# Kernel optimization log

Measured on AMD Instinct MI355X. Metric: run time of the kernel, lower is better.

Reference implementation:

```python
import jax, jax.numpy as jnp
import numpy as np

POOL = 7        # pool_size
NUM_ROIS = 128  # num_rois
WINDOW = 4      # window_size


def setup_inputs() -> dict:
    key = jax.random.key(0)
    k1, k2 = jax.random.split(key)
    img = jax.random.normal(k1, (16, 28, 28, 512), dtype=jnp.float32)
    rois = jax.random.uniform(k2, (16, NUM_ROIS * 5), dtype=jnp.float32)
    return {"img": img, "rois": rois}


def _crop_and_resize(image, boxes, crop):
    """tf.image.crop_and_resize (bilinear, extrapolation_value=0) on a single image.
    image: (H, W, C); boxes: (N, 4) normalized (y1, x1, y2, x2). Returns (N, crop, crop, C)."""
    H, W, C = image.shape
    dt = image.dtype
    y1, x1, y2, x2 = boxes[:, 0], boxes[:, 1], boxes[:, 2], boxes[:, 3]
    i = jnp.arange(crop, dtype=dt)
    # sample grid (crop > 1 branch of TF crop_and_resize)
    ys = y1[:, None] * (H - 1) + i[None, :] * ((y2 - y1) * (H - 1) / (crop - 1))[:, None]  # (N, crop)
    xs = x1[:, None] * (W - 1) + i[None, :] * ((x2 - x1) * (W - 1) / (crop - 1))[:, None]  # (N, crop)
    y0f = jnp.floor(ys)
    x0f = jnp.floor(xs)
    ly = ys - y0f  # fractional weights
    lx = xs - x0f
    y0 = jnp.clip(y0f, 0, H - 1).astype(jnp.int32)
    y1i = jnp.clip(y0f + 1, 0, H - 1).astype(jnp.int32)
    x0 = jnp.clip(x0f, 0, W - 1).astype(jnp.int32)
    x1i = jnp.clip(x0f + 1, 0, W - 1).astype(jnp.int32)
    g = lambda yi, xi: image[yi[:, :, None], xi[:, None, :], :]  # (N, crop, crop, C) gather
    tl, tr, bl, br = g(y0, x0), g(y0, x1i), g(y1i, x0), g(y1i, x1i)
    lxb = lx[:, None, :, None]
    lyb = ly[:, :, None, None]
    val = (tl + (tr - tl) * lxb) * (1 - lyb) + (bl + (br - bl) * lxb) * lyb
    # out-of-range samples -> extrapolation_value = 0
    vy = (ys >= 0) & (ys <= H - 1)
    vx = (xs >= 0) & (xs <= W - 1)
    mask = (vy[:, :, None, None] & vx[:, None, :, None]).astype(dt)
    return val * mask


def reference(img, rois):
    B, H, W, C = img.shape  # H=W=28, C=512 per the layer's hardcoded reshape
    r = rois.reshape(-1, 5)[:, 3:]  # (B*num_rois, 2): columns 3,4 -> x1, y1
    x1 = r[:, 0]
    y1 = r[:, 1]
    x2 = x1 + WINDOW / W  # window_size / cols
    y2 = y1 + WINDOW / H  # window_size / rows
    boxes = jnp.stack([y1, x1, y2, x2], axis=-1)  # (B*num_rois, 4)
    # Original tiles img num_rois times but sets box_ind = zeros, so every crop
    # samples from batch element 0's feature map. Reproduce that exactly.
    crops = _crop_and_resize(img[0], boxes, POOL)  # (B*num_rois, POOL, POOL, C)
    return crops.reshape(B, POOL, POOL, NUM_ROIS * C)
```

## Files before the change

### kernel.cpp

```cpp
#include <hip/hip_runtime.h>

#define POOLSZ 7
#define IMG_H  28
#define IMG_W  28
#define IMG_C  512
#define C4     128
#define SLICES 4
#define SC4    (C4 / SLICES)
#define TOT_ROIS 2048
#define PATCH  6

typedef float f4 __attribute__((ext_vector_type(4)));

__global__ __launch_bounds__(256)
void roi_crop_resize_lds(const float* __restrict__ img,
                         const float* __restrict__ rois,
                         float* __restrict__ out) {
    __shared__ f4 lds[PATCH * PATCH * SC4];

    int n     = blockIdx.x >> 2;
    int slice = blockIdx.x & 3;

    float x1 = rois[n * 5 + 3];
    float y1 = rois[n * 5 + 4];
    float x2 = x1 + 4.0f / 28.0f;
    float y2 = y1 + 4.0f / 28.0f;
    const float Hm1 = 27.0f, Wm1 = 27.0f;
    float dy  = (y2 - y1) * Hm1 / 6.0f;
    float dx  = (x2 - x1) * Wm1 / 6.0f;
    float ys0 = y1 * Hm1;
    float xs0 = x1 * Wm1;

    int Y0 = (int)floorf(ys0); if (Y0 > 27) Y0 = 27; if (Y0 < 0) Y0 = 0;
    int X0 = (int)floorf(xs0); if (X0 > 27) X0 = 27; if (X0 < 0) X0 = 0;

    const f4* img4 = (const f4*)img;
    int tid = threadIdx.x;

    for (int i = tid; i < PATCH * PATCH * SC4; i += 256) {
        int c   = i & (SC4 - 1);
        int pix = i >> 5;
        int ry  = Y0 + pix / PATCH; if (ry > 27) ry = 27;
        int rx  = X0 + pix % PATCH; if (rx > 27) rx = 27;
        lds[i] = img4[(ry * IMG_W + rx) * C4 + slice * SC4 + c];
    }
    __syncthreads();

    f4* out4 = (f4*)out;
    for (int i = tid; i < 49 * SC4; i += 256) {
        int c  = i & (SC4 - 1);
        int p  = i >> 5;
        int py = p / POOLSZ, px = p % POOLSZ;

        float ys = ys0 + (float)py * dy;
        float xs = xs0 + (float)px * dx;
        float y0f = floorf(ys), x0f = floorf(xs);
        float ly = ys - y0f, lx = xs - x0f;
        int y0  = (int)fminf(fmaxf(y0f,       0.f), Hm1);
        int y1i = (int)fminf(fmaxf(y0f + 1.f, 0.f), Hm1);
        int x0  = (int)fminf(fmaxf(x0f,       0.f), Wm1);
        int x1i = (int)fminf(fmaxf(x0f + 1.f, 0.f), Wm1);
        float m = ((ys >= 0.f) & (ys <= Hm1) & (xs >= 0.f) & (xs <= Wm1)) ? 1.f : 0.f;

        int ry0 = y0  - Y0, ry1 = y1i - Y0;
        int rx0 = x0  - X0, rx1 = x1i - X0;
        f4 tl = lds[(ry0 * PATCH + rx0) * SC4 + c];
        f4 tr = lds[(ry0 * PATCH + rx1) * SC4 + c];
        f4 bl = lds[(ry1 * PATCH + rx0) * SC4 + c];
        f4 br = lds[(ry1 * PATCH + rx1) * SC4 + c];

        float omly = 1.f - ly;
        f4 v = ((tl + (tr - tl) * lx) * omly + (bl + (br - bl) * lx) * ly) * m;

        int pos = n * 49 + p;
        __builtin_nontemporal_store(v, out4 + pos * C4 + slice * SC4 + c);
    }
}

extern "C" void kernel_launch(void* const* d_in, const int* in_sizes, int n_in,
                              void* d_out, int out_size, void* d_ws, size_t ws_size,
                              hipStream_t stream) {
    const float* img  = (const float*)d_in[0];
    const float* rois = (const float*)d_in[1];
    float* out = (float*)d_out;

    roi_crop_resize_lds<<<TOT_ROIS * SLICES, 256, 0, stream>>>(img, rois, out);
}
```

Baseline: 217.3 us.

## Precompute bilinear descriptors in LDS and widen channel slice per block

Each block now handles half of an ROI's channels instead of a quarter, halving the number of blocks and the repeated per-ROI setup. The 49 sample positions' patch offsets and combined bilinear weights are computed once into shared memory, so the main loop does four LDS reads and a weighted sum per element. The larger patch buffer raises LDS use per block, which may limit occupancy.

```diff
diff --git a/kernel.cpp b/kernel.cpp
--- a/kernel.cpp
+++ b/kernel.cpp
@@ -5,21 +5,24 @@
 #define IMG_W  28
 #define IMG_C  512
 #define C4     128
-#define SLICES 4
-#define SC4    (C4 / SLICES)
+#define HALF4  64
+#define PATCH  6
+#define NPIX   (PATCH * PATCH)
 #define TOT_ROIS 2048
-#define PATCH  6
 
 typedef float f4 __attribute__((ext_vector_type(4)));
 
-__global__ __launch_bounds__(256)
-void roi_crop_resize_lds(const float* __restrict__ img,
-                         const float* __restrict__ rois,
-                         float* __restrict__ out) {
-    __shared__ f4 lds[PATCH * PATCH * SC4];
+struct __align__(16) Desc { int o0, o1, o2, o3; float w0, w1, w2, w3; };
 
-    int n     = blockIdx.x >> 2;
-    int slice = blockIdx.x & 3;
+__global__ __launch_bounds__(256, 4)
+void roi_crop_resize_v2(const float* __restrict__ img,
+                        const float* __restrict__ rois,
+                        float* __restrict__ out) {
+    __shared__ f4   patch[NPIX * HALF4];
+    __shared__ Desc desc[49];
+
+    int n    = blockIdx.x >> 1;
+    int half = blockIdx.x & 1;
 
     float x1 = rois[n * 5 + 3];
     float y1 = rois[n * 5 + 4];
@@ -35,23 +38,19 @@
     int X0 = (int)floorf(xs0); if (X0 > 27) X0 = 27; if (X0 < 0) X0 = 0;
 
     const f4* img4 = (const f4*)img;
-    int tid = threadIdx.x;
+    int tid   = threadIdx.x;
+    int cbase = half * HALF4;
 
-    for (int i = tid; i < PATCH * PATCH * SC4; i += 256) {
-        int c   = i & (SC4 - 1);
-        int pix = i >> 5;
+    for (int i = tid; i < NPIX * HALF4; i += 256) {
+        int c   = i & (HALF4 - 1);
+        int pix = i >> 6;
         int ry  = Y0 + pix / PATCH; if (ry > 27) ry = 27;
         int rx  = X0 + pix % PATCH; if (rx > 27) rx = 27;
-        lds[i] = img4[(ry * IMG_W + rx) * C4 + slice * SC4 + c];
+        patch[i] = img4[(ry * IMG_W + rx) * C4 + cbase + c];
     }
-    __syncthreads();
 
-    f4* out4 = (f4*)out;
-    for (int i = tid; i < 49 * SC4; i += 256) {
-        int c  = i & (SC4 - 1);
-        int p  = i >> 5;
-        int py = p / POOLSZ, px = p % POOLSZ;
-
+    if (tid < 49) {
+        int py = tid / POOLSZ, px = tid % POOLSZ;
         float ys = ys0 + (float)py * dy;
         float xs = xs0 + (float)px * dx;
         float y0f = floorf(ys), x0f = floorf(xs);
@@ -64,16 +63,33 @@
 
         int ry0 = y0  - Y0, ry1 = y1i - Y0;
         int rx0 = x0  - X0, rx1 = x1i - X0;
-        f4 tl = lds[(ry0 * PATCH + rx0) * SC4 + c];
-        f4 tr = lds[(ry0 * PATCH + rx1) * SC4 + c];
-        f4 bl = lds[(ry1 * PATCH + rx0) * SC4 + c];
-        f4 br = lds[(ry1 * PATCH + rx1) * SC4 + c];
+        float omlx = 1.f - lx, omly = 1.f - ly;
 
-        float omly = 1.f - ly;
-        f4 v = ((tl + (tr - tl) * lx) * omly + (bl + (br - bl) * lx) * ly) * m;
+        Desc d;
+        d.o0 = (ry0 * PATCH + rx0) * HALF4;
+        d.o1 = (ry0 * PATCH + rx1) * HALF4;
+        d.o2 = (ry1 * PATCH + rx0) * HALF4;
+        d.o3 = (ry1 * PATCH + rx1) * HALF4;
+        d.w0 = omlx * omly * m;
+        d.w1 = lx   * omly * m;
+        d.w2 = omlx * ly   * m;
+        d.w3 = lx   * ly   * m;
+        desc[tid] = d;
+    }
+    __syncthreads();
 
-        int pos = n * 49 + p;
-        __builtin_nontemporal_store(v, out4 + pos * C4 + slice * SC4 + c);
+    f4* out4 = (f4*)out;
+    int outBase = n * 49 * C4 + cbase;
+    for (int i = tid; i < 49 * HALF4; i += 256) {
+        int c = i & (HALF4 - 1);
+        int p = i >> 6;
+        Desc d = desc[p];
+        f4 tl = patch[d.o0 + c];
+        f4 tr = patch[d.o1 + c];
+        f4 bl = patch[d.o2 + c];
+        f4 br = patch[d.o3 + c];
+        f4 v = tl * d.w0 + tr * d.w1 + bl * d.w2 + br * d.w3;
+        __builtin_nontemporal_store(v, out4 + outBase + p * C4 + c);
     }
 }
 
@@ -84,5 +100,5 @@
     const float* rois = (const float*)d_in[1];
     float* out = (float*)d_out;
 
-    roi_crop_resize_lds<<<TOT_ROIS * SLICES, 256, 0, stream>>>(img, rois, out);
+    roi_crop_resize_v2<<<TOT_ROIS * 2, 256, 0, stream>>>(img, rois, out);
 }
```

Result: no change. 219.3 us (+0.9%).
